# Kernel optimization log

Hardware: AMD Instinct MI355X
Metric: run time of the kernel (lower is better)

## Reference

```python
import jax, jax.numpy as jnp
import numpy as np

HIDDEN = 4096
N_HEADS = 32
N_KV_HEADS = 8
HEAD_DIM = HIDDEN // N_HEADS  # 128
N_REP = N_HEADS // N_KV_HEADS  # 4
ROPE_THETA = 10000.0
B, S = 2, 2048


def setup_inputs() -> dict:
    key = jax.random.key(0)
    ks = jax.random.split(key, 9)
    sc = 1.0 / np.sqrt(HIDDEN)
    query = jax.random.normal(ks[0], (B, S, HIDDEN), jnp.float32)
    key_t = jax.random.normal(ks[1], (B, S, HIDDEN), jnp.float32)
    value = jax.random.normal(ks[2], (B, S, HIDDEN), jnp.float32)
    position_ids = jnp.sort(jax.random.randint(ks[3], (B, S), 0, S), axis=-1)
    Wq = jax.random.normal(ks[4], (HIDDEN, N_HEADS * HEAD_DIM), jnp.float32) * sc
    Wk = jax.random.normal(ks[5], (HIDDEN, N_KV_HEADS * HEAD_DIM), jnp.float32) * sc
    Wv = jax.random.normal(ks[6], (HIDDEN, N_KV_HEADS * HEAD_DIM), jnp.float32) * sc
    Wo = jax.random.normal(ks[7], (N_HEADS * HEAD_DIM, HIDDEN), jnp.float32) * sc
    return {"query": query, "key": key_t, "value": value,
            "position_ids": position_ids,
            "Wq": Wq, "Wk": Wk, "Wv": Wv, "Wo": Wo}


def _rotate_half(x):
    x1, x2 = jnp.split(x, 2, axis=-1)
    return jnp.concatenate((-x2, x1), axis=-1)


def _rope_cos_sin(position_ids):
    # inv_freq: [head_dim/2]
    inv_freq = 1.0 / (ROPE_THETA ** (jnp.arange(0, HEAD_DIM, 2, dtype=jnp.float32) / HEAD_DIM))
    # freqs: [B, S, head_dim/2] via per-position lookup (equiv. to cache gather cos_cached[position_ids])
    freqs = position_ids[..., None].astype(jnp.float32) * inv_freq
    emb = jnp.concatenate((freqs, freqs), axis=-1)          # [B, S, head_dim]
    return jnp.cos(emb)[:, None, :, :], jnp.sin(emb)[:, None, :, :]  # [B,1,S,hd]


def reference(query, key, value, position_ids, Wq, Wk, Wv, Wo):
    nb, q_len, _ = query.shape
    # QKV projections (bias-free linear)
    q = jnp.einsum('bse,ef->bsf', query, Wq).reshape(nb, q_len, N_HEADS, HEAD_DIM).transpose(0, 2, 1, 3)
    k = jnp.einsum('bse,ef->bsf', key, Wk).reshape(nb, q_len, N_KV_HEADS, HEAD_DIM).transpose(0, 2, 1, 3)
    v = jnp.einsum('bse,ef->bsf', value, Wv).reshape(nb, q_len, N_KV_HEADS, HEAD_DIM).transpose(0, 2, 1, 3)
    # RoPE
    cos, sin = _rope_cos_sin(position_ids)
    q = q * cos + _rotate_half(q) * sin
    k = k * cos + _rotate_half(k) * sin
    # GQA repeat_kv: [B, kvH, S, d] -> [B, H, S, d]
    k = jnp.repeat(k, N_REP, axis=1)
    v = jnp.repeat(v, N_REP, axis=1)
    # scaled dot-product attention (flash-attn semantics, no padding mask)
    scale = 1.0 / jnp.sqrt(jnp.asarray(HEAD_DIM, q.dtype))
    scores = jnp.einsum('bhqd,bhkd->bhqk', q, k) * scale
    probs = jax.nn.softmax(scores, axis=-1)
    ctx = jnp.einsum('bhqk,bhkd->bhqd', probs, v)
    ctx = ctx.transpose(0, 2, 1, 3).reshape(nb, q_len, N_HEADS * HEAD_DIM)
    return jnp.einsum('bsf,fe->bse', ctx, Wo)
```

## Files before the change

kernel.cpp:

```cpp
#include <hip/hip_runtime.h>
#include <hip/hip_bf16.h>

typedef __attribute__((ext_vector_type(8))) short bf16x8;
typedef __attribute__((ext_vector_type(4))) float f32x4;
typedef __attribute__((ext_vector_type(16))) float f32x16;
typedef __attribute__((ext_vector_type(2))) unsigned uint2x;

#define AS1(p) ((const __attribute__((address_space(1))) void*)(p))
#define AS3(p) ((__attribute__((address_space(3))) void*)(p))

__device__ inline unsigned cvtpk_bf16(float lo, float hi) {
  unsigned r;
  asm("v_cvt_pk_bf16_f32 %0, %1, %2" : "=v"(r) : "v"(lo), "v"(hi));
  return r;
}

__device__ inline uint2x plswap(unsigned a, unsigned b) {
  return __builtin_amdgcn_permlane32_swap(a, b, false, false);
}

__global__ __launch_bounds__(256) void prep(const float* __restrict__ Wq,
                                            const float* __restrict__ Wo,
                                            const float* __restrict__ Wk,
                                            const float* __restrict__ Wv,
                                            const float* __restrict__ q_in,
                                            __hip_bfloat16* __restrict__ WqT,
                                            __hip_bfloat16* __restrict__ WoT,
                                            __hip_bfloat16* __restrict__ WkT,
                                            __hip_bfloat16* __restrict__ WvT,
                                            __hip_bfloat16* __restrict__ qc) {
  const int z = blockIdx.z;
  if (z == 4) {
    const size_t b0 = (size_t)blockIdx.x * 4096;
#pragma unroll
    for (int c = 0; c < 4; ++c) {
      const size_t i = b0 + c * 1024 + threadIdx.x * 4;
      float4 v = *(const float4*)(q_in + i);
      union { __hip_bfloat16 h[4]; ushort4 u; } o;
      o.h[0] = __float2bfloat16(v.x);
      o.h[1] = __float2bfloat16(v.y);
      o.h[2] = __float2bfloat16(v.z);
      o.h[3] = __float2bfloat16(v.w);
      *(ushort4*)(qc + i) = o.u;
    }
    return;
  }
  const int N = (z < 2) ? 4096 : 1024;
  const int n0 = (blockIdx.x & 63) << 6;
  if (n0 >= N) return;
  const int k0 = (blockIdx.x >> 6) << 6;
  const float* W = (z == 0) ? Wq : (z == 1) ? Wo : (z == 2) ? Wk : Wv;
  __hip_bfloat16* WT = (z == 0) ? WqT : (z == 1) ? WoT : (z == 2) ? WkT : WvT;
  __shared__ float t[64][68];
  const int tx = threadIdx.x & 15, ty = threadIdx.x >> 4;
#pragma unroll
  for (int j = 0; j < 4; ++j) {
    const int k = ty + j * 16;
    float4 v = *(const float4*)(W + (size_t)(k0 + k) * N + n0 + tx * 4);
    t[tx * 4 + 0][k] = v.x;
    t[tx * 4 + 1][k] = v.y;
    t[tx * 4 + 2][k] = v.z;
    t[tx * 4 + 3][k] = v.w;
  }
  __syncthreads();
#pragma unroll
  for (int j = 0; j < 4; ++j) {
    const int n = ty + j * 16;
    float4 v = *(const float4*)(&t[n][tx * 4]);
    union { __hip_bfloat16 h[4]; ushort4 u; } o;
    o.h[0] = __float2bfloat16(v.x);
    o.h[1] = __float2bfloat16(v.y);
    o.h[2] = __float2bfloat16(v.z);
    o.h[3] = __float2bfloat16(v.w);
    *(ushort4*)(WT + (size_t)(n0 + n) * 4096 + k0 + tx * 4) = o.u;
  }
}

__global__ __launch_bounds__(256) void xconv_kv(const float* __restrict__ k_in,
                                                const float* __restrict__ v_in,
                                                __hip_bfloat16* __restrict__ kc,
                                                __hip_bfloat16* __restrict__ vc) {
  const float* in = blockIdx.y ? v_in : k_in;
  __hip_bfloat16* out = blockIdx.y ? vc : kc;
  size_t i = ((size_t)blockIdx.x * 256 + threadIdx.x) * 4;
  float4 v = *(const float4*)(in + i);
  union { __hip_bfloat16 h[4]; ushort4 u; } o;
  o.h[0] = __float2bfloat16(v.x);
  o.h[1] = __float2bfloat16(v.y);
  o.h[2] = __float2bfloat16(v.z);
  o.h[3] = __float2bfloat16(v.w);
  *(ushort4*)(out + i) = o.u;
}


__device__ inline int tile_off(int row, int k) {
  return (((row >> 4) << 1) + (k >> 5)) * 512 + (row & 15) * 32 +
         ((k & 31) ^ ((row & 8) << 1));
}

__device__ inline void stageA(const __hip_bfloat16* __restrict__ src, int ld, int row0,
                              int kt, int h, __hip_bfloat16* ldsT, int w, int lane) {
#pragma unroll
  for (int li = 0; li < 2; ++li) {
    const int t = li * 8 + w;
    const int grp = ((t >> 3) << 1) + h;
    const int srl = (t & 7) >> 1, sk = t & 1;
    const int rowbase = grp * 64 + srl * 16;
    __hip_bfloat16* dst = ldsT + ((((rowbase >> 4) << 1) + sk) << 9);
    const int r = lane >> 2;
    const int ku = (lane & 3) ^ ((r & 8) >> 2);
    __builtin_amdgcn_global_load_lds(
        AS1(src + (size_t)(row0 + rowbase + r) * ld + kt + (sk << 5) + (ku << 3)),
        AS3(dst), 16, 0, 0);
  }
}

__device__ inline void stageB(const __hip_bfloat16* __restrict__ src, int ld, int col0,
                              int kt, int h, __hip_bfloat16* ldsT, int w, int lane) {
#pragma unroll
  for (int li = 0; li < 2; ++li) {
    const int t = li * 8 + w;
    const int q = t >> 2;
    const int srl = (t >> 1) & 1, sk = t & 1;
    const int colbase = q * 64 + h * 32 + srl * 16;
    __hip_bfloat16* dst = ldsT + ((((colbase >> 4) << 1) + sk) << 9);
    const int r = lane >> 2;
    const int ku = (lane & 3) ^ ((r & 8) >> 2);
    __builtin_amdgcn_global_load_lds(
        AS1(src + (size_t)(col0 + colbase + r) * ld + kt + (sk << 5) + (ku << 3)),
        AS3(dst), 16, 0, 0);
  }
}

template <int OUT_F32>
__global__ __launch_bounds__(512, 1) void gemm256(const __hip_bfloat16* __restrict__ A,
                                                  const __hip_bfloat16* __restrict__ BT,
                                                  void* __restrict__ Cout,
                                                  int M, int N, int K) {
  __shared__ __align__(16) __hip_bfloat16 lds[2][2][16384];
  const int tid = threadIdx.x;
  const int lane = tid & 63, w = tid >> 6;
  const int l15 = lane & 15, lg = lane >> 4;
  const int wm = w >> 2, wn = w & 3;
  const int nbx = N >> 8;
  const int nwg = (M >> 8) * nbx;
  const int bid = blockIdx.x;
  const int swz = (bid & 7) * (nwg >> 3) + (bid >> 3);
  const int m0 = (swz / nbx) << 8, n0 = (swz % nbx) << 8;

  f32x4 acc[8][4] = {};
  const int NT = K >> 6;

  stageA(A, K, m0, 0, 0, &lds[0][0][0], w, lane);
  stageB(BT, K, n0, 0, 0, &lds[0][1][0], w, lane);
  stageA(A, K, m0, 0, 1, &lds[0][0][0], w, lane);
  stageB(BT, K, n0, 0, 1, &lds[0][1][0], w, lane);
  stageA(A, K, m0, 64, 0, &lds[1][0][0], w, lane);
  stageB(BT, K, n0, 64, 0, &lds[1][1][0], w, lane);
  asm volatile("s_waitcnt vmcnt(4)" ::: "memory");
  __builtin_amdgcn_s_barrier();

  for (int j = 0; j < NT; ++j) {
    const int buf = j & 1;
    const __hip_bfloat16* Ab = &lds[buf][0][0];
    const __hip_bfloat16* Bb = &lds[buf][1][0];
    __hip_bfloat16* An = &lds[buf ^ 1][0][0];
    __hip_bfloat16* Bn = &lds[buf ^ 1][1][0];
    __hip_bfloat16* Ac = &lds[buf][0][0];
    __hip_bfloat16* Bc = &lds[buf][1][0];
    const int kt1 = (j + 1) << 6, kt2 = (j + 2) << 6;
    const bool s1 = (j + 1) < NT, s2 = (j + 2) < NT;

    auto phase = [&](int rq, int cq, int sid) {
      bf16x8 af[2][4], bfr[2][2];
#pragma unroll
      for (int kk = 0; kk < 2; ++kk) {
#pragma unroll
        for (int rf = 0; rf < 4; ++rf)
          af[kk][rf] = *(const bf16x8*)(Ab +
              tile_off(wm * 128 + (rq * 4 + rf) * 16 + l15, kk * 32 + lg * 8));
#pragma unroll
        for (int cf = 0; cf < 2; ++cf)
          bfr[kk][cf] = *(const bf16x8*)(Bb +
              tile_off(wn * 64 + (cq * 2 + cf) * 16 + l15, kk * 32 + lg * 8));
      }
      if (sid == 0)      { if (s1) stageA(A, K, m0, kt1, 1, An, w, lane); }
      else if (sid == 1) { if (s1) stageB(BT, K, n0, kt1, 1, Bn, w, lane); }
      else if (sid == 2) { if (s2) stageA(A, K, m0, kt2, 0, Ac, w, lane); }
      else {
        if (s2) stageB(BT, K, n0, kt2, 0, Bc, w, lane);
        if (s2) asm volatile("s_waitcnt vmcnt(4)" ::: "memory");
        else    asm volatile("s_waitcnt vmcnt(0)" ::: "memory");
      }
      __builtin_amdgcn_s_barrier();
      asm volatile("s_waitcnt lgkmcnt(0)" ::: "memory");
      __builtin_amdgcn_sched_barrier(0);
      __builtin_amdgcn_s_setprio(1);
#pragma unroll
      for (int kk = 0; kk < 2; ++kk)
#pragma unroll
        for (int rf = 0; rf < 4; ++rf)
#pragma unroll
          for (int cf = 0; cf < 2; ++cf)
            acc[rq * 4 + rf][cq * 2 + cf] = __builtin_amdgcn_mfma_f32_16x16x32_bf16(
                af[kk][rf], bfr[kk][cf], acc[rq * 4 + rf][cq * 2 + cf], 0, 0, 0);
      __builtin_amdgcn_s_setprio(0);
      __builtin_amdgcn_s_barrier();
    };
    phase(0, 0, 0);
    phase(0, 1, 1);
    phase(1, 0, 2);
    phase(1, 1, 3);
  }

#pragma unroll
  for (int rf = 0; rf < 8; ++rf)
#pragma unroll
    for (int cf = 0; cf < 4; ++cf)
#pragma unroll
      for (int i = 0; i < 4; ++i) {
        const size_t row = (size_t)(m0 + wm * 128 + rf * 16 + lg * 4 + i);
        const size_t col = (size_t)(n0 + wn * 64 + cf * 16 + l15);
        if (OUT_F32)
          ((float*)Cout)[row * N + col] = acc[rf][cf][i];
        else
          ((__hip_bfloat16*)Cout)[row * N + col] = __float2bfloat16(acc[rf][cf][i]);
      }
}

__global__ __launch_bounds__(512, 1) void gemm_kv8(const __hip_bfloat16* __restrict__ Ak,
                                                   const __hip_bfloat16* __restrict__ Av,
                                                   const __hip_bfloat16* __restrict__ BkT,
                                                   const __hip_bfloat16* __restrict__ BvT,
                                                   const int* __restrict__ pos,
                                                   __hip_bfloat16* __restrict__ Kp,
                                                   __hip_bfloat16* __restrict__ VT) {
  __shared__ __align__(16) __hip_bfloat16 lds[2][24576];
  const int zz = blockIdx.z;
  const __hip_bfloat16* A  = zz ? Av : Ak;
  const __hip_bfloat16* BT = zz ? BvT : BkT;
  const int K = 4096;
  const int tid = threadIdx.x;
  const int lane = tid & 63, w = tid >> 6;
  const int l15 = lane & 15, lg = lane >> 4;
  const int wm = w >> 2, wn = w & 3;
  const int bid = blockIdx.x;
  const int swz = (bid & 7) * 16 + (bid >> 3);
  const int m0 = (swz >> 2) << 7;
  const int n0 = (swz & 3) << 8;

  auto stgA = [&](int kt, int h, __hip_bfloat16* ldsA) {
    const int r16 = 2 * h + ((w >> 2) << 2) + ((w >> 1) & 1);
    const int sk = w & 1;
    __hip_bfloat16* dst = ldsA + (((r16 << 1) + sk) << 9);
    const int r = lane >> 2;
    const int ku = (lane & 3) ^ ((r & 8) >> 2);
    __builtin_amdgcn_global_load_lds(
        AS1(A + (size_t)(m0 + r16 * 16 + r) * K + kt + (sk << 5) + (ku << 3)),
        AS3(dst), 16, 0, 0);
  };
  auto stgB = [&](int kt, int h, __hip_bfloat16* ldsB) {
#pragma unroll
    for (int li = 0; li < 2; ++li) {
      const int idx = li * 8 + w;
      const int r16 = ((idx >> 2) << 2) + 2 * h + ((idx >> 1) & 1);
      const int sk = idx & 1;
      __hip_bfloat16* dst = ldsB + (((r16 << 1) + sk) << 9);
      const int r = lane >> 2;
      const int ku = (lane & 3) ^ ((r & 8) >> 2);
      __builtin_amdgcn_global_load_lds(
          AS1(BT + (size_t)(n0 + r16 * 16 + r) * K + kt + (sk << 5) + (ku << 3)),
          AS3(dst), 16, 0, 0);
    }
  };

  f32x4 acc[4][4] = {};
  const int NT = K >> 6;

  stgA(0, 0, &lds[0][0]);
  stgB(0, 0, &lds[0][8192]);
  stgA(0, 1, &lds[0][0]);
  stgB(0, 1, &lds[0][8192]);
  stgA(64, 0, &lds[1][0]);
  stgB(64, 0, &lds[1][8192]);
  asm volatile("s_waitcnt vmcnt(3)" ::: "memory");
  __builtin_amdgcn_s_barrier();

  for (int j = 0; j < NT; ++j) {
    const int buf = j & 1;
    const __hip_bfloat16* Ab = &lds[buf][0];
    const __hip_bfloat16* Bb = &lds[buf][8192];
    __hip_bfloat16* An = &lds[buf ^ 1][0];
    __hip_bfloat16* Bn = &lds[buf ^ 1][8192];
    __hip_bfloat16* Ac = &lds[buf][0];
    __hip_bfloat16* Bc = &lds[buf][8192];
    const int kt1 = (j + 1) << 6, kt2 = (j + 2) << 6;
    const bool s1 = (j + 1) < NT, s2 = (j + 2) < NT;

    auto phase = [&](int rq, int cq, int sid) {
      bf16x8 af[2][2], bfr[2][2];
#pragma unroll
      for (int kk = 0; kk < 2; ++kk) {
#pragma unroll
        for (int rf = 0; rf < 2; ++rf)
          af[kk][rf] = *(const bf16x8*)(Ab +
              tile_off(wm * 64 + (rq * 2 + rf) * 16 + l15, kk * 32 + lg * 8));
#pragma unroll
        for (int cf = 0; cf < 2; ++cf)
          bfr[kk][cf] = *(const bf16x8*)(Bb +
              tile_off(wn * 64 + (cq * 2 + cf) * 16 + l15, kk * 32 + lg * 8));
      }
      if (sid == 0)      { if (s1) stgA(kt1, 1, An); }
      else if (sid == 1) { if (s1) stgB(kt1, 1, Bn); }
      else if (sid == 2) { if (s2) stgA(kt2, 0, Ac); }
      else {
        if (s2) stgB(kt2, 0, Bc);
        if (s2) asm volatile("s_waitcnt vmcnt(3)" ::: "memory");
        else    asm volatile("s_waitcnt vmcnt(0)" ::: "memory");
      }
      __builtin_amdgcn_s_barrier();
      asm volatile("s_waitcnt lgkmcnt(0)" ::: "memory");
      __builtin_amdgcn_sched_barrier(0);
      __builtin_amdgcn_s_setprio(1);
#pragma unroll
      for (int kk = 0; kk < 2; ++kk)
#pragma unroll
        for (int rf = 0; rf < 2; ++rf)
#pragma unroll
          for (int cf = 0; cf < 2; ++cf)
            acc[rq * 2 + rf][cq * 2 + cf] = __builtin_amdgcn_mfma_f32_16x16x32_bf16(
                af[kk][rf], bfr[kk][cf], acc[rq * 2 + rf][cq * 2 + cf], 0, 0, 0);
      __builtin_amdgcn_s_setprio(0);
      __builtin_amdgcn_s_barrier();
    };
    phase(0, 0, 0);
    phase(0, 1, 1);
    phase(1, 0, 2);
    phase(1, 1, 3);
  }

  if (zz == 0) {
    __syncthreads();
    __hip_bfloat16* T = &lds[0][0];
    const int TS = 264;
#pragma unroll
    for (int rf = 0; rf < 4; ++rf)
#pragma unroll
      for (int cf = 0; cf < 4; ++cf)
#pragma unroll
        for (int i = 0; i < 4; ++i)
          T[(wm * 64 + rf * 16 + lg * 4 + i) * TS + wn * 64 + cf * 16 + l15] =
              __float2bfloat16(acc[rf][cf][i]);
    __syncthreads();
    const int row = tid >> 2, quad = tid & 3;
    const int gr = m0 + row;
    const float p = (float)pos[gr];
#pragma unroll
    for (int qb = 0; qb < 4; ++qb) {
      const int bi = quad + qb * 4;
      const int hl = bi >> 3, jb = (bi & 7) * 8;
      bf16x8 lo  = *(const bf16x8*)&T[row * TS + hl * 128 + jb];
      bf16x8 hi8 = *(const bf16x8*)&T[row * TS + hl * 128 + jb + 64];
      union { __hip_bfloat16 h[8]; bf16x8 v; } o0, o1;
#pragma unroll
      for (int e = 0; e < 8; ++e) {
        const int j = jb + e;
        const float fr = p * exp2f((float)j * -0.2076205059304601f);
        float sn, cs;
        __sincosf(fr, &sn, &cs);
        const float x0 = __uint_as_float(((unsigned)(unsigned short)lo[e]) << 16);
        const float x1 = __uint_as_float(((unsigned)(unsigned short)hi8[e]) << 16);
        o0.h[e] = __float2bfloat16(x0 * cs - x1 * sn);
        o1.h[e] = __float2bfloat16(x1 * cs + x0 * sn);
      }
      *(bf16x8*)(Kp + (size_t)gr * 1024 + n0 + hl * 128 + jb)      = o0.v;
      *(bf16x8*)(Kp + (size_t)gr * 1024 + n0 + hl * 128 + jb + 64) = o1.v;
    }
  } else {
    const int b = m0 >> 11, s0g = m0 & 2047;
#pragma unroll
    for (int rf = 0; rf < 4; ++rf)
#pragma unroll
      for (int cf = 0; cf < 4; ++cf) {
        const int d = n0 + wn * 64 + cf * 16 + l15;
        const int g = d >> 7, dl = d & 127;
        const int srow = s0g + wm * 64 + rf * 16 + lg * 4;
        union { __hip_bfloat16 h[4]; unsigned long long u; } pkv;
#pragma unroll
        for (int i = 0; i < 4; ++i) pkv.h[i] = __float2bfloat16(acc[rf][cf][i]);
        *(unsigned long long*)(VT + ((size_t)(b * 8 + g) * 128 + dl) * 2048 + srow) = pkv.u;
      }
  }
}

__global__ __launch_bounds__(512) void attn(const __hip_bfloat16* __restrict__ Q,
                                            const __hip_bfloat16* __restrict__ Kp,
                                            const __hip_bfloat16* __restrict__ VT,
                                            const int* __restrict__ pos,
                                            __hip_bfloat16* __restrict__ ctx,
                                            float qs) {
  const int tid = threadIdx.x;
  const int lane = tid & 63, w = tid >> 6;
  const int l31 = lane & 31, hi = lane >> 5;
  const int qt = blockIdx.x, h = blockIdx.y, b = blockIdx.z;
  const int kvh = h >> 2;
  const int q0 = qt * 256 + w * 32;

  const __hip_bfloat16* Qh = Q + (size_t)(b * 2048) * 4096 + h * 128;
  const __hip_bfloat16* Kh = Kp + (size_t)(b * 2048) * 1024 + kvh * 128;
  const __hip_bfloat16* Vh = VT + (size_t)(b * 8 + kvh) * 128 * 2048;

  __shared__ __hip_bfloat16 Ks[2][64 * 128];
  __shared__ __hip_bfloat16 Vs[2][128 * 64];

  auto stage = [&](int buf, int s0) {
#pragma unroll
    for (int j = 0; j < 2; ++j) {
      const int idx = w * 64 + lane + j * 512;
      const int rK = idx >> 4, uK = idx & 15;
      __builtin_amdgcn_global_load_lds(
          AS1(Kh + (size_t)(s0 + rK) * 1024 + ((uK ^ (rK & 7)) << 3)),
          AS3(&Ks[buf][(w * 64 + j * 512) * 8]), 16, 0, 0);
      const int rV = idx >> 3, uV = idx & 7;
      __builtin_amdgcn_global_load_lds(
          AS1(Vh + (size_t)rV * 2048 + s0 + ((uV ^ (rV & 7)) << 3)),
          AS3(&Vs[buf][(w * 64 + j * 512) * 8]), 16, 0, 0);
    }
  };

  stage(0, 0);

  const int qrow = q0 + l31;
  const float pp = (float)pos[b * 2048 + qrow];
  bf16x8 qf[8];
  {
#pragma unroll
    for (int kd = 0; kd < 4; ++kd) {
      bf16x8 rlo = *(const bf16x8*)(Qh + (size_t)qrow * 4096 + kd * 16 + hi * 8);
      bf16x8 rhi = *(const bf16x8*)(Qh + (size_t)qrow * 4096 + (kd + 4) * 16 + hi * 8);
      bf16x8 olo, ohi;
#pragma unroll
      for (int e = 0; e < 8; ++e) {
        const int j = kd * 16 + hi * 8 + e;
        const float fr = pp * exp2f((float)j * -0.2076205059304601f);
        float sn, cs;
        __sincosf(fr, &sn, &cs);
        const float x0 = __uint_as_float(((unsigned)(unsigned short)rlo[e]) << 16);
        const float x1 = __uint_as_float(((unsigned)(unsigned short)rhi[e]) << 16);
        __hip_bfloat16 h0 = __float2bfloat16((x0 * cs - x1 * sn) * qs);
        __hip_bfloat16 h1 = __float2bfloat16((x1 * cs + x0 * sn) * qs);
        olo[e] = *(short*)&h0;
        ohi[e] = *(short*)&h1;
      }
      qf[kd] = olo;
      qf[kd + 4] = ohi;
    }
  }

  bf16x8 ones;
#pragma unroll
  for (int e = 0; e < 8; ++e) ones[e] = (short)0x3F80;

  f32x16 o[4] = {};
  f32x16 ol = {};
  __syncthreads();

  auto tile = [&](int tt, int cur, bool pf) {
    if (pf) stage(cur ^ 1, (tt + 1) * 64);

    f32x16 p[2] = {};
    __builtin_amdgcn_s_setprio(1);
#pragma unroll
    for (int n = 0; n < 2; ++n)
#pragma unroll
      for (int kd = 0; kd < 8; ++kd) {
        const int row = n * 32 + l31;
        bf16x8 kf = *(const bf16x8*)(&Ks[cur][row * 128 + (((2 * kd + hi) ^ (row & 7)) << 3)]);
        p[n] = __builtin_amdgcn_mfma_f32_32x32x16_bf16(kf, qf[kd], p[n], 0, 0, 0);
      }
    __builtin_amdgcn_s_setprio(0);

#pragma unroll
    for (int n = 0; n < 2; ++n)
#pragma unroll
      for (int e = 0; e < 16; ++e) p[n][e] = exp2f(p[n][e]);

    bf16x8 paf[4];
#pragma unroll
    for (int n = 0; n < 2; ++n)
#pragma unroll
      for (int ks = 0; ks < 2; ++ks) {
        const int bse = ks * 8;
        unsigned a1 = cvtpk_bf16(p[n][bse + 0], p[n][bse + 1]);
        unsigned b1 = cvtpk_bf16(p[n][bse + 4], p[n][bse + 5]);
        unsigned a2 = cvtpk_bf16(p[n][bse + 2], p[n][bse + 3]);
        unsigned b2 = cvtpk_bf16(p[n][bse + 6], p[n][bse + 7]);
        uint2x s1 = plswap(a1, b1);
        uint2x s2 = plswap(a2, b2);
        union { unsigned u[4]; bf16x8 v; } pw = {{s1[0], s2[0], s1[1], s2[1]}};
        paf[n * 2 + ks] = pw.v;
      }

    __builtin_amdgcn_s_setprio(1);
#pragma unroll
    for (int slot = 0; slot < 4; ++slot) {
      ol = __builtin_amdgcn_mfma_f32_32x32x16_bf16(ones, paf[slot], ol, 0, 0, 0);
#pragma unroll
      for (int dc = 0; dc < 4; ++dc) {
        const int row = dc * 32 + l31;
        bf16x8 vf = *(const bf16x8*)(&Vs[cur][row * 64 + (((2 * slot + hi) ^ (row & 7)) << 3)]);
        o[dc] = __builtin_amdgcn_mfma_f32_32x32x16_bf16(vf, paf[slot], o[dc], 0, 0, 0);
      }
    }
    __builtin_amdgcn_s_setprio(0);
    __syncthreads();
  };

  for (int t2 = 0; t2 < 16; ++t2) {
    tile(2 * t2, 0, true);
    tile(2 * t2 + 1, 1, t2 < 15);
  }

  const float inv = 1.0f / ol[0];
  const size_t rowbase = ((size_t)(b * 2048 + q0 + l31)) * 4096 + h * 128;
#pragma unroll
  for (int dc = 0; dc < 4; ++dc)
#pragma unroll
    for (int g = 0; g < 4; ++g) {
      union { unsigned short us[4]; ushort4 u4; } pk;
#pragma unroll
      for (int e = 0; e < 4; ++e) {
        __hip_bfloat16 hv = __float2bfloat16(o[dc][g * 4 + e] * inv);
        pk.us[e] = *(unsigned short*)&hv;
      }
      *(ushort4*)(ctx + rowbase + dc * 32 + g * 8 + hi * 4) = pk.u4;
    }
}


extern "C" void kernel_launch(void* const* d_in, const int* in_sizes, int n_in,
                              void* d_out, int out_size, void* d_ws, size_t ws_size,
                              hipStream_t stream) {
  const float* q_in = (const float*)d_in[0];
  const float* k_in = (const float*)d_in[1];
  const float* v_in = (const float*)d_in[2];
  const int* pos    = (const int*)d_in[3];
  const float* Wq   = (const float*)d_in[4];
  const float* Wk   = (const float*)d_in[5];
  const float* Wv   = (const float*)d_in[6];
  const float* Wo   = (const float*)d_in[7];

  char* ws = (char*)d_ws;
  __hip_bfloat16* xbuf = (__hip_bfloat16*)(ws);
  __hip_bfloat16* WqT  = (__hip_bfloat16*)(ws + 33554432);
  __hip_bfloat16* WkT  = (__hip_bfloat16*)(ws + 67108864);
  __hip_bfloat16* WvT  = (__hip_bfloat16*)(ws + 75497472);
  __hip_bfloat16* WoT  = (__hip_bfloat16*)(ws + 83886080);
  __hip_bfloat16* Qp   = (__hip_bfloat16*)(ws + 117440512);
  __hip_bfloat16* Kp   = (__hip_bfloat16*)(ws + 150994944);
  __hip_bfloat16* VTb  = (__hip_bfloat16*)(ws + 167772160);
  __hip_bfloat16* vconv = WqT;

  prep<<<dim3(4096, 1, 5), 256, 0, stream>>>(Wq, Wo, Wk, Wv, q_in,
                                             WqT, WoT, WkT, WvT, xbuf);
  gemm256<0><<<256, 512, 0, stream>>>(xbuf, WqT, Qp, 4096, 4096, 4096);
  xconv_kv<<<dim3(16384, 2), 256, 0, stream>>>(k_in, v_in, xbuf, vconv);
  gemm_kv8<<<dim3(128, 1, 2), 512, 0, stream>>>(xbuf, vconv, WkT, WvT, pos, Kp, VTb);
  attn<<<dim3(8, 32, 2), 512, 0, stream>>>(Qp, Kp, VTb, pos, xbuf,
                                           0.08838834764831845f * 1.4426950408889634f);
  gemm256<1><<<256, 512, 0, stream>>>(xbuf, WoT, d_out, 4096, 4096, 4096);
}
```

Measured before the change: 607.8 us.

## Triple-buffer K tiles and use explicit vmcnt waits in attention loop

Splits the K/V staging into separate loaders, adds a third K buffer so K is prefetched two tiles ahead while V is prefetched one ahead, and replaces __syncthreads with explicit s_waitcnt vmcnt counts plus raw barriers. The intent is to keep more global-to-LDS loads in flight and stop waiting on the newest prefetch before computing the current tile. It uses more LDS, which may lower occupancy. It also depends on hand-counted vmcnt values matching the compiler's load ordering, so a miscount could cause data races.

Result: slower. 624.2 us (+2.7%).

```diff
diff --git a/kernel.cpp b/kernel.cpp
--- a/kernel.cpp
+++ b/kernel.cpp
@@ -410,25 +410,29 @@
   const __hip_bfloat16* Kh = Kp + (size_t)(b * 2048) * 1024 + kvh * 128;
   const __hip_bfloat16* Vh = VT + (size_t)(b * 8 + kvh) * 128 * 2048;
 
-  __shared__ __hip_bfloat16 Ks[2][64 * 128];
+  __shared__ __hip_bfloat16 Ks[3][64 * 128];
   __shared__ __hip_bfloat16 Vs[2][128 * 64];
 
-  auto stage = [&](int buf, int s0) {
-#pragma unroll
-    for (int j = 0; j < 2; ++j) {
-      const int idx = w * 64 + lane + j * 512;
+  auto stageK = [&](int buf, int s0) {
+#pragma unroll
+    for (int jj = 0; jj < 2; ++jj) {
+      const int idx = w * 64 + lane + jj * 512;
       const int rK = idx >> 4, uK = idx & 15;
       __builtin_amdgcn_global_load_lds(
           AS1(Kh + (size_t)(s0 + rK) * 1024 + ((uK ^ (rK & 7)) << 3)),
-          AS3(&Ks[buf][(w * 64 + j * 512) * 8]), 16, 0, 0);
+          AS3(&Ks[buf][(w * 64 + jj * 512) * 8]), 16, 0, 0);
+    }
+  };
+  auto stageV = [&](int buf, int s0) {
+#pragma unroll
+    for (int jj = 0; jj < 2; ++jj) {
+      const int idx = w * 64 + lane + jj * 512;
       const int rV = idx >> 3, uV = idx & 7;
       __builtin_amdgcn_global_load_lds(
           AS1(Vh + (size_t)rV * 2048 + s0 + ((uV ^ (rV & 7)) << 3)),
-          AS3(&Vs[buf][(w * 64 + j * 512) * 8]), 16, 0, 0);
+          AS3(&Vs[buf][(w * 64 + jj * 512) * 8]), 16, 0, 0);
     }
   };
-
-  stage(0, 0);
 
   const int qrow = q0 + l31;
   const float pp = (float)pos[b * 2048 + qrow];
@@ -461,12 +465,24 @@
 #pragma unroll
   for (int e = 0; e < 8; ++e) ones[e] = (short)0x3F80;
 
+  stageV(0, 0);
+  stageK(0, 0);
+  stageK(1, 64);
+
   f32x16 o[4] = {};
   f32x16 ol = {};
-  __syncthreads();
-
-  auto tile = [&](int tt, int cur, bool pf) {
-    if (pf) stage(cur ^ 1, (tt + 1) * 64);
+
+  int kcur = 0;
+  for (int j = 0; j < 32; ++j) {
+    const int vcur = j & 1;
+    const int knx2 = (kcur >= 1) ? kcur - 1 : 2;
+
+    if (j + 1 < 32) stageV(vcur ^ 1, (j + 1) * 64);
+    if (j + 2 < 32) stageK(knx2, (j + 2) * 64);
+    if (j < 30)       asm volatile("s_waitcnt vmcnt(6)" ::: "memory");
+    else if (j == 30) asm volatile("s_waitcnt vmcnt(4)" ::: "memory");
+    else              asm volatile("s_waitcnt vmcnt(0)" ::: "memory");
+    __builtin_amdgcn_s_barrier();
 
     f32x16 p[2] = {};
     __builtin_amdgcn_s_setprio(1);
@@ -475,7 +491,7 @@
 #pragma unroll
       for (int kd = 0; kd < 8; ++kd) {
         const int row = n * 32 + l31;
-        bf16x8 kf = *(const bf16x8*)(&Ks[cur][row * 128 + (((2 * kd + hi) ^ (row & 7)) << 3)]);
+        bf16x8 kf = *(const bf16x8*)(&Ks[kcur][row * 128 + (((2 * kd + hi) ^ (row & 7)) << 3)]);
         p[n] = __builtin_amdgcn_mfma_f32_32x32x16_bf16(kf, qf[kd], p[n], 0, 0, 0);
       }
     __builtin_amdgcn_s_setprio(0);
@@ -508,17 +524,13 @@
 #pragma unroll
       for (int dc = 0; dc < 4; ++dc) {
         const int row = dc * 32 + l31;
-        bf16x8 vf = *(const bf16x8*)(&Vs[cur][row * 64 + (((2 * slot + hi) ^ (row & 7)) << 3)]);
+        bf16x8 vf = *(const bf16x8*)(&Vs[vcur][row * 64 + (((2 * slot + hi) ^ (row & 7)) << 3)]);
         o[dc] = __builtin_amdgcn_mfma_f32_32x32x16_bf16(vf, paf[slot], o[dc], 0, 0, 0);
       }
     }
     __builtin_amdgcn_s_setprio(0);
-    __syncthreads();
-  };
-
-  for (int t2 = 0; t2 < 16; ++t2) {
-    tile(2 * t2, 0, true);
-    tile(2 * t2 + 1, 1, t2 < 15);
+    __builtin_amdgcn_s_barrier();
+    kcur = (kcur == 2) ? 0 : kcur + 1;
   }
 
   const float inv = 1.0f / ol[0];
```
